# Optimization experiments

Measured on AMD Instinct MI355X. Metric: run time of the kernel, lower is better.

The kernel has to match this reference:

```python
import jax, jax.numpy as jnp
import numpy as np

B, N, DIM = 4, 1024, 768
H, HD = 12, DIM // 12
GP = 49
MLP = 3072


def _layernorm(x, w, b, eps=1e-5):
    mu = x.mean(axis=-1, keepdims=True)
    var = ((x - mu) ** 2).mean(axis=-1, keepdims=True)
    return (x - mu) * jax.lax.rsqrt(var + eps) * w + b


def setup_inputs() -> dict:
    key = jax.random.key(0)
    ks = jax.random.split(key, 12)
    s = 0.02
    return {
        "x": jax.random.normal(ks[0], (B, N, DIM), jnp.float32),
        "ln1_w": jnp.ones((DIM,), jnp.float32),
        "ln1_b": jnp.zeros((DIM,), jnp.float32),
        "qkv_w": jax.random.normal(ks[1], (DIM, 3 * DIM), jnp.float32) * s,
        "qkv_b": jnp.zeros((3 * DIM,), jnp.float32),
        "proj_w": jax.random.normal(ks[2], (DIM, DIM), jnp.float32) * s,
        "proj_b": jnp.zeros((DIM,), jnp.float32),
        "gp_w": jax.random.normal(ks[3], (GP, DIM), jnp.float32) * s,  # nn.Linear(dim, gp_num).weight, shape (gp_num, dim)
        "alpha": jax.random.normal(ks[4], (1, H, 1, 1), jnp.float32),
        "ln2_w": jnp.ones((DIM,), jnp.float32),
        "ln2_b": jnp.zeros((DIM,), jnp.float32),
        "ff1_w": jax.random.normal(ks[5], (DIM, MLP), jnp.float32) * s,
        "ff1_b": jnp.zeros((MLP,), jnp.float32),
        "ff2_w": jax.random.normal(ks[6], (MLP, DIM), jnp.float32) * s,
        "ff2_b": jnp.zeros((DIM,), jnp.float32),
    }


def reference(x, ln1_w, ln1_b, qkv_w, qkv_b, proj_w, proj_b, gp_w, alpha,
              ln2_w, ln2_b, ff1_w, ff1_b, ff2_w, ff2_b):
    b, n, _ = x.shape
    # --- attention branch ---
    xn = _layernorm(x, ln1_w, ln1_b)
    qkv = xn @ qkv_w + qkv_b                                 # [b,n,3*dim]
    q, k, v = jnp.split(qkv, 3, axis=-1)
    to_heads = lambda t: t.reshape(b, n, H, HD).transpose(0, 2, 1, 3)  # [b,h,n,hd]
    q, k, v = to_heads(q), to_heads(k), to_heads(v)
    scale = HD ** -0.5
    attn = jnp.einsum('bhnd,bhmd->bhnm', q, k) * scale       # raw scores
    # group weights: view (gp_num, dim) -> (h, gp_num, hd) (row-major, same as torch .view)
    gp = gp_w.reshape(H, GP, HD)
    gw = jnp.einsum('bhnd,hmd->bhnm', v, gp)                 # [b,h,n,gp]
    gw = jax.nn.gelu(gw, approximate=False)
    gw = jax.nn.softmax(gw, axis=-1)
    gw = jnp.einsum('bhnm,bhkm->bhnk', gw, gw)               # [b,h,n,n]
    attn = jax.nn.softmax(attn * gw, axis=-1)
    a = jax.nn.sigmoid(alpha)
    attn = (1.0 - a) * attn + a * gw
    attn = attn / (attn.sum(axis=2, keepdims=True) + 1e-8)   # note: dim=2 (column renorm), faithful to source
    out = jnp.einsum('bhnm,bhmd->bhnd', attn, v)
    out = out.transpose(0, 2, 1, 3).reshape(b, n, DIM)
    out = out @ proj_w + proj_b
    x = out + x
    # --- FFN branch ---
    xn = _layernorm(x, ln2_w, ln2_b)
    hdn = jax.nn.gelu(xn @ ff1_w + ff1_b, approximate=False)
    x = (hdn @ ff2_w + ff2_b) + x
    return x
```

## Files before the change

kernel.cpp:

```cpp
#include <hip/hip_runtime.h>
#include <hip/hip_bf16.h>
#include <math.h>

#define DEVI __device__ __forceinline__

typedef __bf16 bf16x8 __attribute__((ext_vector_type(8)));
typedef float f32x4 __attribute__((ext_vector_type(4)));
typedef unsigned int u32x4 __attribute__((ext_vector_type(4)));
typedef float f32x4v __attribute__((ext_vector_type(4)));
typedef unsigned short u16;

DEVI u16 f2bf(float f) {
    __hip_bfloat16 h = __float2bfloat16(f);
    return __builtin_bit_cast(u16, h);
}
DEVI float bf2f(u16 u) {
    unsigned int x = ((unsigned int)u) << 16;
    return __builtin_bit_cast(float, x);
}
DEVI float gelu_f(float x) {
    float y = 0.7978845608f * (x + 0.044715f * x * x * x);
    float e = __expf(2.f * y);
    float t = 1.f - 2.f / (e + 1.f);
    return 0.5f * x * (1.f + t);
}
DEVI float sigm(float x) { return 1.f / (1.f + __expf(-x)); }

DEVI bf16x8 ldfrag(const u16* p) {
    return __builtin_bit_cast(bf16x8, *reinterpret_cast<const u32x4*>(p));
}

DEVI void gload_lds16(const u16* g, u16* l) {
    __builtin_amdgcn_global_load_lds(
        (const __attribute__((address_space(1))) void*)g,
        (__attribute__((address_space(3))) void*)l, 16, 0, 0);
}

DEVI void stage8(const u16* gbase, long long stride, u16* lds, int lane) {
    int r = lane >> 3;
    int kg = (lane & 7) ^ r;
    gload_lds16(gbase + (long long)r * stride + kg * 8, lds);
}
DEVI bf16x8 fragsw(const u16* tile, int rr, int k) {
    return ldfrag(&tile[rr * 64 + ((k ^ (rr & 7)) << 3)]);
}

__global__ __launch_bounds__(256) void zero_k(float* __restrict__ p) {
    p[(long long)blockIdx.x * 256 + threadIdx.x] = 0.f;
}

__global__ __launch_bounds__(256) void tcast_k(const float* __restrict__ in, u16* __restrict__ out,
                                               int R, int C) {
    __shared__ float tile[32][33];
    int c0 = blockIdx.x * 32, r0 = blockIdx.y * 32;
    for (int ry = threadIdx.y; ry < 32; ry += 8)
        tile[ry][threadIdx.x] = in[(long long)(r0 + ry) * C + c0 + threadIdx.x];
    __syncthreads();
    for (int cy = threadIdx.y; cy < 32; cy += 8)
        out[(long long)(c0 + cy) * R + r0 + threadIdx.x] = f2bf(tile[threadIdx.x][cy]);
}

__global__ __launch_bounds__(256) void ln_k(const float* __restrict__ parts, int nparts, long long pstride,
                                            const float* __restrict__ bias2, const float* __restrict__ in2,
                                            const float* __restrict__ w, const float* __restrict__ b,
                                            u16* __restrict__ outbf, float* __restrict__ x1out) {
    int row = blockIdx.x;
    long long ro = (long long)row * 768;
    __shared__ float lds1[4], lds2[4];
    float v[3];
    float s = 0.f, sq = 0.f;
#pragma unroll
    for (int j = 0; j < 3; j++) {
        int c = threadIdx.x + j * 256;
        float x = 0.f;
        for (int p = 0; p < nparts; p++) x += parts[p * pstride + ro + c];
        if (bias2) x += bias2[c];
        if (in2) x += in2[ro + c];
        v[j] = x; s += x; sq += x * x;
    }
    if (x1out) {
#pragma unroll
        for (int j = 0; j < 3; j++) x1out[ro + threadIdx.x + j * 256] = v[j];
    }
    for (int off = 32; off; off >>= 1) { s += __shfl_down(s, off); sq += __shfl_down(sq, off); }
    int wid = threadIdx.x >> 6;
    if ((threadIdx.x & 63) == 0) { lds1[wid] = s; lds2[wid] = sq; }
    __syncthreads();
    s = lds1[0] + lds1[1] + lds1[2] + lds1[3];
    sq = lds2[0] + lds2[1] + lds2[2] + lds2[3];
    float mu = s * (1.f / 768.f);
    float var = sq * (1.f / 768.f) - mu * mu;
    float rs = rsqrtf(var + 1e-5f);
#pragma unroll
    for (int j = 0; j < 3; j++) {
        int c = threadIdx.x + j * 256;
        outbf[ro + c] = f2bf((v[j] - mu) * rs * w[c] + b[c]);
    }
}

struct GemmP {
    const u16* A; const u16* B;
    float* outF; u16* outB;
    const float* bias;
    u16* qh; u16* kh; u16* vh;
    int K, lda, ldb, ldc;
    long long pstride;
    int epi;
    int splits;
};

__global__ __launch_bounds__(256) void gemm_bt4(GemmP p) {
    __shared__ u16 As[128 * 64];
    __shared__ u16 Bs[128 * 64];
    const int tid = threadIdx.x, lane = tid & 63, wave = tid >> 6;
    const int l16 = lane & 15, qd = lane >> 4;
    const int bn0 = blockIdx.x * 128, bm0 = blockIdx.y * 128;
    const int wm0 = (wave >> 1) * 64, wn0 = (wave & 1) * 64;
    const int kc = p.K / p.splits;
    const int kbeg = blockIdx.z * kc, kend = kbeg + kc;
    f32x4 acc[4][4] = {};
    for (int k0 = kbeg; k0 < kend; k0 += 64) {
        __syncthreads();
#pragma unroll
        for (int t = 0; t < 4; t++) {
            int rowg = wave * 32 + t * 8;
            stage8(p.A + (long long)(bm0 + rowg) * p.lda + k0, p.lda, As + rowg * 64, lane);
            stage8(p.B + (long long)(bn0 + rowg) * p.ldb + k0, p.ldb, Bs + rowg * 64, lane);
        }
        __syncthreads();
#pragma unroll
        for (int s = 0; s < 2; s++) {
            bf16x8 af[4], bv[4];
#pragma unroll
            for (int i = 0; i < 4; i++) af[i] = fragsw(As, wm0 + i * 16 + l16, s * 4 + qd);
#pragma unroll
            for (int j = 0; j < 4; j++) bv[j] = fragsw(Bs, wn0 + j * 16 + l16, s * 4 + qd);
#pragma unroll
            for (int i = 0; i < 4; i++)
#pragma unroll
                for (int j = 0; j < 4; j++)
                    acc[i][j] = __builtin_amdgcn_mfma_f32_16x16x32_bf16(af[i], bv[j], acc[i][j], 0, 0, 0);
        }
    }
#pragma unroll
    for (int i = 0; i < 4; i++)
#pragma unroll
        for (int j = 0; j < 4; j++)
#pragma unroll
            for (int r = 0; r < 4; r++) {
                int row = bm0 + wm0 + i * 16 + qd * 4 + r;
                int col = bn0 + wn0 + j * 16 + l16;
                float v = acc[i][j][r];
                if (p.epi == 0) {
                    p.outF[(long long)blockIdx.z * p.pstride + (long long)row * p.ldc + col] = v;
                } else if (p.epi == 2) {
                    p.outB[(long long)row * p.ldc + col] = f2bf(gelu_f(v + p.bias[col]));
                } else {
                    v += p.bias[col];
                    int sect = col / 768, cc = col % 768;
                    int h = cc >> 6, d = cc & 63;
                    int b = row >> 10, n = row & 1023;
                    long long o = ((long long)(b * 12 + h) * 1024 + n) * 64 + d;
                    if (sect == 0) p.qh[o] = f2bf(v * 0.125f);
                    else if (sect == 1) p.kh[o] = f2bf(v);
                    else p.vh[o] = f2bf(v);
                }
            }
}

__global__ __launch_bounds__(256) void gpcast_k(const float* __restrict__ gp_w, u16* __restrict__ gpB) {
    int h = blockIdx.x;
    for (int i = threadIdx.x; i < 4096; i += 256) {
        int m = i >> 6, d = i & 63;
        float v = (m < 49) ? gp_w[h * 3136 + m * 64 + d] : 0.f;
        gpB[h * 4096 + i] = f2bf(v);
    }
}

__global__ __launch_bounds__(256) void gw0m_k(const u16* __restrict__ vh, const u16* __restrict__ gpB,
                                              u16* __restrict__ gwn) {
    __shared__ u16 As[64 * 64];
    __shared__ u16 Bs[64 * 64];
    const int tid = threadIdx.x, lane = tid & 63, wave = tid >> 6;
    const int l16 = lane & 15, qd = lane >> 4;
    const int z = blockIdx.y, n0 = blockIdx.x * 64, h = z % 12;
    const u16* vz = vh + ((long long)z * 1024 + n0) * 64;
    const u16* gz = gpB + h * 4096;
#pragma unroll
    for (int t = 0; t < 2; t++) {
        int rowg = wave * 16 + t * 8;
        stage8(vz + (long long)rowg * 64, 64, As + rowg * 64, lane);
        stage8(gz + (long long)rowg * 64, 64, Bs + rowg * 64, lane);
    }
    __syncthreads();
    f32x4 acc[4] = {};
#pragma unroll
    for (int s = 0; s < 2; s++) {
        bf16x8 af = fragsw(As, wave * 16 + l16, s * 4 + qd);
#pragma unroll
        for (int j = 0; j < 4; j++) {
            bf16x8 bv = fragsw(Bs, j * 16 + l16, s * 4 + qd);
            acc[j] = __builtin_amdgcn_mfma_f32_16x16x32_bf16(af, bv, acc[j], 0, 0, 0);
        }
    }
    float ex[4][4];
#pragma unroll
    for (int r = 0; r < 4; r++) {
        float mx = -1e30f;
        float gv[4];
#pragma unroll
        for (int j = 0; j < 4; j++) {
            int col = j * 16 + l16;
            float g = gelu_f(acc[j][r]);
            gv[j] = g;
            if (col < 49) mx = fmaxf(mx, g);
            else gv[j] = -1e30f;
        }
        mx = fmaxf(mx, __shfl_xor(mx, 1)); mx = fmaxf(mx, __shfl_xor(mx, 2));
        mx = fmaxf(mx, __shfl_xor(mx, 4)); mx = fmaxf(mx, __shfl_xor(mx, 8));
        float s = 0.f;
#pragma unroll
        for (int j = 0; j < 4; j++) {
            int col = j * 16 + l16;
            float e = (col < 49) ? __expf(gv[j] - mx) : 0.f;
            ex[r][j] = e;
            s += e;
        }
        s += __shfl_xor(s, 1); s += __shfl_xor(s, 2);
        s += __shfl_xor(s, 4); s += __shfl_xor(s, 8);
        float inv = 1.f / s;
        int row = wave * 16 + qd * 4 + r;
        long long o = ((long long)z * 1024 + n0 + row) * 64;
#pragma unroll
        for (int j = 0; j < 4; j++)
            gwn[o + j * 16 + l16] = f2bf(ex[r][j] * inv);
    }
}

__global__ __launch_bounds__(256) void attn_tg4(const u16* __restrict__ qh, const u16* __restrict__ kh,
                                                const u16* __restrict__ gwn, u16* __restrict__ e,
                                                float* __restrict__ rowsumE) {
    __shared__ u16 As[128 * 64];
    __shared__ u16 Bs[128 * 64];
    const int tid = threadIdx.x, lane = tid & 63, wave = tid >> 6;
    const int l16 = lane & 15, qd = lane >> 4;
    const int bn0 = blockIdx.x * 128, bm0 = blockIdx.y * 128, z = blockIdx.z;
    const int wm0 = (wave >> 1) * 64, wn0 = (wave & 1) * 64;
    const u16* qz = qh + (long long)z * 65536;
    const u16* kz = kh + (long long)z * 65536;
    const u16* gz = gwn + (long long)z * 65536;
    f32x4 accS[4][4] = {};
    f32x4 accG[4][4] = {};
#pragma unroll
    for (int t = 0; t < 4; t++) {
        int rowg = wave * 32 + t * 8;
        stage8(qz + (long long)(bm0 + rowg) * 64, 64, As + rowg * 64, lane);
        stage8(kz + (long long)(bn0 + rowg) * 64, 64, Bs + rowg * 64, lane);
    }
    __syncthreads();
#pragma unroll
    for (int s = 0; s < 2; s++) {
        bf16x8 af[4], bv[4];
#pragma unroll
        for (int i = 0; i < 4; i++) af[i] = fragsw(As, wm0 + i * 16 + l16, s * 4 + qd);
#pragma unroll
        for (int j = 0; j < 4; j++) bv[j] = fragsw(Bs, wn0 + j * 16 + l16, s * 4 + qd);
#pragma unroll
        for (int i = 0; i < 4; i++)
#pragma unroll
            for (int j = 0; j < 4; j++)
                accS[i][j] = __builtin_amdgcn_mfma_f32_16x16x32_bf16(af[i], bv[j], accS[i][j], 0, 0, 0);
    }
    __syncthreads();
#pragma unroll
    for (int t = 0; t < 4; t++) {
        int rowg = wave * 32 + t * 8;
        stage8(gz + (long long)(bm0 + rowg) * 64, 64, As + rowg * 64, lane);
        stage8(gz + (long long)(bn0 + rowg) * 64, 64, Bs + rowg * 64, lane);
    }
    __syncthreads();
#pragma unroll
    for (int s = 0; s < 2; s++) {
        bf16x8 af[4], bv[4];
#pragma unroll
        for (int i = 0; i < 4; i++) af[i] = fragsw(As, wm0 + i * 16 + l16, s * 4 + qd);
#pragma unroll
        for (int j = 0; j < 4; j++) bv[j] = fragsw(Bs, wn0 + j * 16 + l16, s * 4 + qd);
#pragma unroll
        for (int i = 0; i < 4; i++)
#pragma unroll
            for (int j = 0; j < 4; j++)
                accG[i][j] = __builtin_amdgcn_mfma_f32_16x16x32_bf16(af[i], bv[j], accG[i][j], 0, 0, 0);
    }
    long long zoff = (long long)z * 1048576;
#pragma unroll
    for (int i = 0; i < 4; i++)
#pragma unroll
        for (int r = 0; r < 4; r++) {
            int row = bm0 + wm0 + i * 16 + qd * 4 + r;
            float rs = 0.f;
#pragma unroll
            for (int j = 0; j < 4; j++) {
                int col = bn0 + wn0 + j * 16 + l16;
                float ev = __expf(accS[i][j][r] * accG[i][j][r]);
                e[zoff + (long long)row * 1024 + col] = f2bf(ev);
                rs += ev;
            }
            rs += __shfl_xor(rs, 1); rs += __shfl_xor(rs, 2);
            rs += __shfl_xor(rs, 4); rs += __shfl_xor(rs, 8);
            if (l16 == 0) atomicAdd(&rowsumE[z * 1024 + row], rs);
        }
}

__global__ __launch_bounds__(256) void combine2_k(const u16* __restrict__ gwn, const float* __restrict__ alpha,
                                                  float* __restrict__ colsum) {
    int z = blockIdx.x, h = z % 12;
    int j = threadIdx.x & 63, part = threadIdx.x >> 6;
    __shared__ float lds[4][64];
    __shared__ float Sl[64];
    float s = 0.f;
    for (int i = 0; i < 256; i++)
        s += bf2f(gwn[((long long)z * 1024 + part * 256 + i) * 64 + j]);
    lds[part][j] = s;
    __syncthreads();
    if (threadIdx.x < 64)
        Sl[threadIdx.x] = lds[0][threadIdx.x] + lds[1][threadIdx.x] + lds[2][threadIdx.x] + lds[3][threadIdx.x];
    __syncthreads();
    float a = sigm(alpha[h]);
    for (int m = threadIdx.x; m < 1024; m += 256) {
        const u16* g = gwn + ((long long)z * 1024 + m) * 64;
        float dot = 0.f;
#pragma unroll 8
        for (int jj = 0; jj < 64; jj++) dot += bf2f(g[jj]) * Sl[jj];
        colsum[z * 1024 + m] = a * dot;
    }
}

__global__ __launch_bounds__(256) void colsumE_k(const u16* __restrict__ e, const float* __restrict__ rowsumE,
                                                 const float* __restrict__ alpha, float* __restrict__ colsum) {
    int m = blockIdx.x * 256 + threadIdx.x;
    int n0 = blockIdx.y * 128;
    int z = blockIdx.z, h = z % 12;
    float a = sigm(alpha[h]);
    const u16* p = e + (long long)z * 1048576;
    const float* rs = rowsumE + z * 1024;
    float s = 0.f;
    for (int n = n0; n < n0 + 128; n++) s += bf2f(p[(long long)n * 1024 + m]) * (1.f / rs[n]);
    atomicAdd(&colsum[z * 1024 + m], (1.f - a) * s);
}

__global__ __launch_bounds__(256) void vpt_k(const u16* __restrict__ vh, const float* __restrict__ colsum,
                                             u16* __restrict__ vpt) {
    int z = blockIdx.y, m0 = blockIdx.x * 64;
    __shared__ float ts[64 * 65];
    int mi = threadIdx.x >> 6, d = threadIdx.x & 63;
    for (int rr = 0; rr < 16; rr++) {
        int row = rr * 4 + mi;
        ts[row * 65 + d] = bf2f(vh[((long long)z * 1024 + m0 + row) * 64 + d]);
    }
    __syncthreads();
    int mj = threadIdx.x & 63, d0 = threadIdx.x >> 6;
    for (int rr = 0; rr < 16; rr++) {
        int dd = rr * 4 + d0;
        float cs = colsum[z * 1024 + m0 + mj] + 1e-8f;
        vpt[((long long)z * 64 + dd) * 1024 + m0 + mj] = f2bf(ts[mj * 65 + dd] / cs);
    }
}

__global__ __launch_bounds__(256) void wgemm_k(const u16* __restrict__ gwn, const u16* __restrict__ vpt,
                                               float* __restrict__ Wt) {
    int z = blockIdx.y, n0 = blockIdx.x * 128;
    __shared__ u16 gs[128 * 64];
    __shared__ u16 vs2[64 * 128];
    for (int i = threadIdx.x; i < 128 * 64; i += 256) {
        int nn = i >> 6, j = i & 63;
        gs[i] = gwn[((long long)z * 1024 + n0 + nn) * 64 + j];
        int d = i >> 7, n2 = i & 127;
        vs2[i] = vpt[((long long)z * 64 + d) * 1024 + n0 + n2];
    }
    __syncthreads();
    int j = threadIdx.x & 63, dg = threadIdx.x >> 6;
    float acc[16] = {};
    for (int nn = 0; nn < 128; nn++) {
        float g = bf2f(gs[nn * 64 + j]);
#pragma unroll
        for (int i = 0; i < 16; i++) acc[i] += g * bf2f(vs2[(dg * 16 + i) * 128 + nn]);
    }
#pragma unroll
    for (int i = 0; i < 16; i++)
        atomicAdd(&Wt[((long long)z * 64 + dg * 16 + i) * 64 + j], acc[i]);
}

__global__ __launch_bounds__(256) void wtcast_k(const float* __restrict__ Wt, u16* __restrict__ WtB) {
    long long i = (long long)blockIdx.x * 256 + threadIdx.x;
    WtB[i] = f2bf(Wt[i]);
}

__global__ __launch_bounds__(256) void attn_out4(const u16* __restrict__ e, const u16* __restrict__ vpt,
                                                 const u16* __restrict__ gwn, const u16* __restrict__ WtB,
                                                 const float* __restrict__ rowsumE,
                                                 const float* __restrict__ alpha, u16* __restrict__ out) {
    __shared__ u16 As[64 * 64];
    __shared__ u16 Bs[64 * 64];
    const int tid = threadIdx.x, lane = tid & 63, wave = tid >> 6;
    const int l16 = lane & 15, qd = lane >> 4;
    const int bm0 = blockIdx.x * 64, z = blockIdx.y;
    const int h = z % 12, b = z / 12;
    const u16* Pz = e + (long long)z * 1048576;
    const u16* vz = vpt + (long long)z * 65536;
    const int wr = wave * 16;
    f32x4 accP[4] = {};
    f32x4 accG[4] = {};
    for (int k0 = 0; k0 < 1024; k0 += 64) {
        __syncthreads();
#pragma unroll
        for (int t = 0; t < 2; t++) {
            int rowg = wave * 16 + t * 8;
            stage8(Pz + (long long)(bm0 + rowg) * 1024 + k0, 1024, As + rowg * 64, lane);
            stage8(vz + (long long)rowg * 1024 + k0, 1024, Bs + rowg * 64, lane);
        }
        __syncthreads();
#pragma unroll
        for (int s = 0; s < 2; s++) {
            bf16x8 af = fragsw(As, wr + l16, s * 4 + qd);
#pragma unroll
            for (int j = 0; j < 4; j++) {
                bf16x8 bv = fragsw(Bs, j * 16 + l16, s * 4 + qd);
                accP[j] = __builtin_amdgcn_mfma_f32_16x16x32_bf16(af, bv, accP[j], 0, 0, 0);
            }
        }
    }
    const u16* gz = gwn + (long long)z * 65536;
    const u16* wz = WtB + (long long)z * 4096;
    __syncthreads();
#pragma unroll
    for (int t = 0; t < 2; t++) {
        int rowg = wave * 16 + t * 8;
        stage8(gz + (long long)(bm0 + rowg) * 64, 64, As + rowg * 64, lane);
        stage8(wz + (long long)rowg * 64, 64, Bs + rowg * 64, lane);
    }
    __syncthreads();
#pragma unroll
    for (int s = 0; s < 2; s++) {
        bf16x8 af = fragsw(As, wr + l16, s * 4 + qd);
#pragma unroll
        for (int j = 0; j < 4; j++) {
            bf16x8 bv = fragsw(Bs, j * 16 + l16, s * 4 + qd);
            accG[j] = __builtin_amdgcn_mfma_f32_16x16x32_bf16(af, bv, accG[j], 0, 0, 0);
        }
    }
    float a = sigm(alpha[h]);
#pragma unroll
    for (int r = 0; r < 4; r++) {
        int n = bm0 + wr + qd * 4 + r;
        float sc = (1.f - a) / rowsumE[z * 1024 + n];
#pragma unroll
        for (int j = 0; j < 4; j++) {
            int d = j * 16 + l16;
            float v = sc * accP[j][r] + a * accG[j][r];
            out[((long long)(b * 1024 + n)) * 768 + h * 64 + d] = f2bf(v);
        }
    }
}

__global__ __launch_bounds__(256) void fuse2_k(const float* __restrict__ parts, long long pstride4,
                                               const float* __restrict__ bias, const float* __restrict__ x1,
                                               float* __restrict__ outp) {
    long long i4 = (long long)blockIdx.x * 256 + threadIdx.x;
    int c4 = (int)(i4 % 192);
    const f32x4v* p0 = (const f32x4v*)parts;
    f32x4v v = p0[i4] + p0[pstride4 + i4];
    f32x4v bb = ((const f32x4v*)bias)[c4];
    f32x4v xx = ((const f32x4v*)x1)[i4];
    ((f32x4v*)outp)[i4] = v + bb + xx;
}

extern "C" void kernel_launch(void* const* d_in, const int* in_sizes, int n_in,
                              void* d_out, int out_size, void* d_ws, size_t ws_size,
                              hipStream_t stream) {
    const float* x      = (const float*)d_in[0];
    const float* ln1_w  = (const float*)d_in[1];
    const float* ln1_b  = (const float*)d_in[2];
    const float* qkv_w  = (const float*)d_in[3];
    const float* qkv_b  = (const float*)d_in[4];
    const float* proj_w = (const float*)d_in[5];
    const float* proj_b = (const float*)d_in[6];
    const float* gp_w   = (const float*)d_in[7];
    const float* alpha  = (const float*)d_in[8];
    const float* ln2_w  = (const float*)d_in[9];
    const float* ln2_b  = (const float*)d_in[10];
    const float* ff1_w  = (const float*)d_in[11];
    const float* ff1_b  = (const float*)d_in[12];
    const float* ff2_w  = (const float*)d_in[13];
    const float* ff2_b  = (const float*)d_in[14];

    char* w = (char*)d_ws;
    size_t off = 0;
    auto alloc = [&](size_t bytes) { size_t r = off; off += (bytes + 255) & ~(size_t)255; return r; };

    u16*   xn_bf   = (u16*)(w + alloc(4096LL * 768 * 2));
    u16*   wqkv_t  = (u16*)(w + alloc(2304LL * 768 * 2));
    u16*   wproj_t = (u16*)(w + alloc(768LL * 768 * 2));
    u16*   wff1_t  = (u16*)(w + alloc(3072LL * 768 * 2));
    u16*   wff2_t  = (u16*)(w + alloc(768LL * 3072 * 2));
    u16*   gpB     = (u16*)(w + alloc(12LL * 64 * 64 * 2));
    u16*   qh      = (u16*)(w + alloc(48LL * 1024 * 64 * 2));
    u16*   kh      = (u16*)(w + alloc(48LL * 1024 * 64 * 2));
    u16*   vh      = (u16*)(w + alloc(48LL * 1024 * 64 * 2));
    u16*   gwn     = (u16*)(w + alloc(48LL * 1024 * 64 * 2));
    u16*   ebuf    = (u16*)(w + alloc(48LL * 1024 * 1024 * 2));
    float* rowsumE = (float*)(w + alloc(48LL * 1024 * 4));
    float* Wt      = (float*)(w + alloc(48LL * 64 * 64 * 4));
    u16*   WtB     = (u16*)(w + alloc(48LL * 64 * 64 * 2));
    float* colsum  = (float*)(w + alloc(48LL * 1024 * 4));
    u16*   vpt     = (u16*)(w + alloc(48LL * 64 * 1024 * 2));
    float* x1      = (float*)(w + alloc(4096LL * 768 * 4));
    u16*   attn_o  = (u16*)(w + alloc(4096LL * 768 * 2));
    u16*   xn2     = (u16*)(w + alloc(4096LL * 768 * 2));
    float* projP = (float*)ebuf;
    u16*   hmid  = (u16*)((char*)ebuf + 2 * 4096LL * 768 * 4);
    float* ff2P  = (float*)((char*)ebuf + 2 * 4096LL * 768 * 4 + 4096LL * 3072 * 2);

    dim3 blk(256);
    const long long PS = 4096LL * 768;

    tcast_k<<<dim3(72, 24), dim3(32, 8), 0, stream>>>(qkv_w, wqkv_t, 768, 2304);
    tcast_k<<<dim3(24, 24), dim3(32, 8), 0, stream>>>(proj_w, wproj_t, 768, 768);
    tcast_k<<<dim3(96, 24), dim3(32, 8), 0, stream>>>(ff1_w, wff1_t, 768, 3072);
    tcast_k<<<dim3(24, 96), dim3(32, 8), 0, stream>>>(ff2_w, wff2_t, 3072, 768);
    gpcast_k<<<dim3(12), blk, 0, stream>>>(gp_w, gpB);

    ln_k<<<dim3(4096), blk, 0, stream>>>(x, 1, 0, nullptr, nullptr, ln1_w, ln1_b, xn_bf, nullptr);

    {
        GemmP p = {xn_bf, wqkv_t, nullptr, nullptr, qkv_b, qh, kh, vh, 768, 768, 768, 0, 0, 4, 1};
        gemm_bt4<<<dim3(18, 32, 1), blk, 0, stream>>>(p);
    }

    gw0m_k<<<dim3(16, 48), blk, 0, stream>>>(vh, gpB, gwn);

    zero_k<<<dim3(192), blk, 0, stream>>>(rowsumE);
    attn_tg4<<<dim3(8, 8, 48), blk, 0, stream>>>(qh, kh, gwn, ebuf, rowsumE);

    combine2_k<<<dim3(48), blk, 0, stream>>>(gwn, alpha, colsum);
    colsumE_k<<<dim3(4, 8, 48), blk, 0, stream>>>(ebuf, rowsumE, alpha, colsum);

    vpt_k<<<dim3(16, 48), blk, 0, stream>>>(vh, colsum, vpt);

    zero_k<<<dim3(768), blk, 0, stream>>>(Wt);
    wgemm_k<<<dim3(8, 48), blk, 0, stream>>>(gwn, vpt, Wt);
    wtcast_k<<<dim3(768), blk, 0, stream>>>(Wt, WtB);

    attn_out4<<<dim3(16, 48), blk, 0, stream>>>(ebuf, vpt, gwn, WtB, rowsumE, alpha, attn_o);

    {
        GemmP p = {attn_o, wproj_t, projP, nullptr, nullptr, nullptr, nullptr, nullptr,
                   768, 768, 768, 768, PS, 0, 2};
        gemm_bt4<<<dim3(6, 32, 2), blk, 0, stream>>>(p);
    }

    ln_k<<<dim3(4096), blk, 0, stream>>>(projP, 2, PS, proj_b, x, ln2_w, ln2_b, xn2, x1);

    {
        GemmP p = {xn2, wff1_t, nullptr, hmid, ff1_b, nullptr, nullptr, nullptr,
                   768, 768, 768, 3072, 0, 2, 1};
        gemm_bt4<<<dim3(24, 32, 1), blk, 0, stream>>>(p);
    }

    {
        GemmP p = {hmid, wff2_t, ff2P, nullptr, nullptr, nullptr, nullptr, nullptr,
                   3072, 3072, 3072, 768, PS, 0, 2};
        gemm_bt4<<<dim3(6, 32, 2), blk, 0, stream>>>(p);
    }

    fuse2_k<<<dim3(3072), blk, 0, stream>>>(ff2P, PS / 4, ff2_b, x1, (float*)d_out);
}
```

Baseline: 480.9 us.

## Shrink GEMM tiles, fold zero-fill and cast kernels, vectorize column sums

Several separate changes are bundled. The bf16 GEMM moves from 128x128 tiles with four waves to 64x128 tiles with two waves, which doubles the block count per launch. The zero-fill kernels for rowsumE and Wt are removed: the zeroing now happens inside ln_k and gw0m_k, and the fp32-to-bf16 Wt cast is done while staging inside attn_out4, which drops three launches. colsumE_k now reads 16-byte vectors and reduces through shared memory before issuing atomics, cutting scalar loads and atomic traffic. The tradeoffs are more duplicated B-tile loads per output in the GEMM and uncoalesced scalar fp32 reads for Wt in attn_out4.

```diff
diff --git a/kernel.cpp b/kernel.cpp
--- a/kernel.cpp
+++ b/kernel.cpp
@@ -43,10 +43,6 @@
 }
 DEVI bf16x8 fragsw(const u16* tile, int rr, int k) {
     return ldfrag(&tile[rr * 64 + ((k ^ (rr & 7)) << 3)]);
-}
-
-__global__ __launch_bounds__(256) void zero_k(float* __restrict__ p) {
-    p[(long long)blockIdx.x * 256 + threadIdx.x] = 0.f;
 }
 
 __global__ __launch_bounds__(256) void tcast_k(const float* __restrict__ in, u16* __restrict__ out,
@@ -63,8 +59,10 @@
 __global__ __launch_bounds__(256) void ln_k(const float* __restrict__ parts, int nparts, long long pstride,
                                             const float* __restrict__ bias2, const float* __restrict__ in2,
                                             const float* __restrict__ w, const float* __restrict__ b,
-                                            u16* __restrict__ outbf, float* __restrict__ x1out) {
+                                            u16* __restrict__ outbf, float* __restrict__ x1out,
+                                            float* __restrict__ zfill) {
     int row = blockIdx.x;
+    if (zfill && row < 192) zfill[row * 256 + threadIdx.x] = 0.f;
     long long ro = (long long)row * 768;
     __shared__ float lds1[4], lds2[4];
     float v[3];
@@ -109,13 +107,13 @@
     int splits;
 };
 
-__global__ __launch_bounds__(256) void gemm_bt4(GemmP p) {
-    __shared__ u16 As[128 * 64];
+__global__ __launch_bounds__(128) void gemm_bt2(GemmP p) {
+    __shared__ u16 As[64 * 64];
     __shared__ u16 Bs[128 * 64];
     const int tid = threadIdx.x, lane = tid & 63, wave = tid >> 6;
     const int l16 = lane & 15, qd = lane >> 4;
-    const int bn0 = blockIdx.x * 128, bm0 = blockIdx.y * 128;
-    const int wm0 = (wave >> 1) * 64, wn0 = (wave & 1) * 64;
+    const int bn0 = blockIdx.x * 128, bm0 = blockIdx.y * 64;
+    const int wn0 = wave * 64;
     const int kc = p.K / p.splits;
     const int kbeg = blockIdx.z * kc, kend = kbeg + kc;
     f32x4 acc[4][4] = {};
@@ -125,6 +123,10 @@
         for (int t = 0; t < 4; t++) {
             int rowg = wave * 32 + t * 8;
             stage8(p.A + (long long)(bm0 + rowg) * p.lda + k0, p.lda, As + rowg * 64, lane);
+        }
+#pragma unroll
+        for (int t = 0; t < 8; t++) {
+            int rowg = wave * 64 + t * 8;
             stage8(p.B + (long long)(bn0 + rowg) * p.ldb + k0, p.ldb, Bs + rowg * 64, lane);
         }
         __syncthreads();
@@ -132,7 +134,7 @@
         for (int s = 0; s < 2; s++) {
             bf16x8 af[4], bv[4];
 #pragma unroll
-            for (int i = 0; i < 4; i++) af[i] = fragsw(As, wm0 + i * 16 + l16, s * 4 + qd);
+            for (int i = 0; i < 4; i++) af[i] = fragsw(As, i * 16 + l16, s * 4 + qd);
 #pragma unroll
             for (int j = 0; j < 4; j++) bv[j] = fragsw(Bs, wn0 + j * 16 + l16, s * 4 + qd);
 #pragma unroll
@@ -148,7 +150,7 @@
         for (int j = 0; j < 4; j++)
 #pragma unroll
             for (int r = 0; r < 4; r++) {
-                int row = bm0 + wm0 + i * 16 + qd * 4 + r;
+                int row = bm0 + i * 16 + qd * 4 + r;
                 int col = bn0 + wn0 + j * 16 + l16;
                 float v = acc[i][j][r];
                 if (p.epi == 0) {
@@ -178,7 +180,11 @@
 }
 
 __global__ __launch_bounds__(256) void gw0m_k(const u16* __restrict__ vh, const u16* __restrict__ gpB,
-                                              u16* __restrict__ gwn) {
+                                              u16* __restrict__ gwn, float* __restrict__ Wt) {
+    {
+        long long zi = ((long long)blockIdx.y * 16 + blockIdx.x) * 256 + threadIdx.x;
+        Wt[zi] = 0.f;
+    }
     __shared__ u16 As[64 * 64];
     __shared__ u16 Bs[64 * 64];
     const int tid = threadIdx.x, lane = tid & 63, wave = tid >> 6;
@@ -338,15 +344,35 @@
 
 __global__ __launch_bounds__(256) void colsumE_k(const u16* __restrict__ e, const float* __restrict__ rowsumE,
                                                  const float* __restrict__ alpha, float* __restrict__ colsum) {
-    int m = blockIdx.x * 256 + threadIdx.x;
+    int z = blockIdx.x, h = z % 12;
     int n0 = blockIdx.y * 128;
-    int z = blockIdx.z, h = z % 12;
-    float a = sigm(alpha[h]);
+    int grp = threadIdx.x & 127;
+    int half = threadIdx.x >> 7;
     const u16* p = e + (long long)z * 1048576;
     const float* rs = rowsumE + z * 1024;
-    float s = 0.f;
-    for (int n = n0; n < n0 + 128; n++) s += bf2f(p[(long long)n * 1024 + m]) * (1.f / rs[n]);
-    atomicAdd(&colsum[z * 1024 + m], (1.f - a) * s);
+    float acc[8] = {};
+    for (int n = n0 + half * 64; n < n0 + half * 64 + 64; n++) {
+        unsigned int rw[4];
+        *reinterpret_cast<u32x4*>(rw) = *reinterpret_cast<const u32x4*>(&p[(long long)n * 1024 + grp * 8]);
+        float inv = 1.f / rs[n];
+#pragma unroll
+        for (int q = 0; q < 4; q++) {
+            float lo = __builtin_bit_cast(float, rw[q] << 16);
+            float hi = __builtin_bit_cast(float, rw[q] & 0xffff0000u);
+            acc[2 * q] += lo * inv;
+            acc[2 * q + 1] += hi * inv;
+        }
+    }
+    __shared__ float part[2][128][8];
+#pragma unroll
+    for (int j = 0; j < 8; j++) part[half][grp][j] = acc[j];
+    __syncthreads();
+    if (half == 0) {
+        float a = sigm(alpha[h]);
+#pragma unroll
+        for (int j = 0; j < 8; j++)
+            atomicAdd(&colsum[z * 1024 + grp * 8 + j], (1.f - a) * (part[0][grp][j] + part[1][grp][j]));
+    }
 }
 
 __global__ __launch_bounds__(256) void vpt_k(const u16* __restrict__ vh, const float* __restrict__ colsum,
@@ -391,13 +417,8 @@
         atomicAdd(&Wt[((long long)z * 64 + dg * 16 + i) * 64 + j], acc[i]);
 }
 
-__global__ __launch_bounds__(256) void wtcast_k(const float* __restrict__ Wt, u16* __restrict__ WtB) {
-    long long i = (long long)blockIdx.x * 256 + threadIdx.x;
-    WtB[i] = f2bf(Wt[i]);
-}
-
 __global__ __launch_bounds__(256) void attn_out4(const u16* __restrict__ e, const u16* __restrict__ vpt,
-                                                 const u16* __restrict__ gwn, const u16* __restrict__ WtB,
+                                                 const u16* __restrict__ gwn, const float* __restrict__ Wt,
                                                  const float* __restrict__ rowsumE,
                                                  const float* __restrict__ alpha, u16* __restrict__ out) {
     __shared__ u16 As[64 * 64];
@@ -431,13 +452,22 @@
         }
     }
     const u16* gz = gwn + (long long)z * 65536;
-    const u16* wz = WtB + (long long)z * 4096;
+    const float* wz = Wt + (long long)z * 4096;
     __syncthreads();
 #pragma unroll
     for (int t = 0; t < 2; t++) {
         int rowg = wave * 16 + t * 8;
         stage8(gz + (long long)(bm0 + rowg) * 64, 64, As + rowg * 64, lane);
-        stage8(wz + (long long)rowg * 64, 64, Bs + rowg * 64, lane);
+    }
+    {
+        int row = tid >> 2, c0 = (tid & 3) * 16;
+        const float* wrow = wz + row * 64;
+#pragma unroll
+        for (int j0 = 0; j0 < 16; j0++) {
+            int j = c0 + j0;
+            int pos = (((j >> 3) ^ (row & 7)) << 3) | (j & 7);
+            Bs[row * 64 + pos] = f2bf(wrow[j]);
+        }
     }
     __syncthreads();
 #pragma unroll
@@ -511,7 +541,6 @@
     u16*   ebuf    = (u16*)(w + alloc(48LL * 1024 * 1024 * 2));
     float* rowsumE = (float*)(w + alloc(48LL * 1024 * 4));
     float* Wt      = (float*)(w + alloc(48LL * 64 * 64 * 4));
-    u16*   WtB     = (u16*)(w + alloc(48LL * 64 * 64 * 2));
     float* colsum  = (float*)(w + alloc(48LL * 1024 * 4));
     u16*   vpt     = (u16*)(w + alloc(48LL * 64 * 1024 * 2));
     float* x1      = (float*)(w + alloc(4096LL * 768 * 4));
@@ -522,6 +551,7 @@
     float* ff2P  = (float*)((char*)ebuf + 2 * 4096LL * 768 * 4 + 4096LL * 3072 * 2);
 
     dim3 blk(256);
+    dim3 blk2(128);
     const long long PS = 4096LL * 768;
 
     tcast_k<<<dim3(72, 24), dim3(32, 8), 0, stream>>>(qkv_w, wqkv_t, 768, 2304);
@@ -530,47 +560,44 @@
     tcast_k<<<dim3(24, 96), dim3(32, 8), 0, stream>>>(ff2_w, wff2_t, 3072, 768);
     gpcast_k<<<dim3(12), blk, 0, stream>>>(gp_w, gpB);
 
-    ln_k<<<dim3(4096), blk, 0, stream>>>(x, 1, 0, nullptr, nullptr, ln1_w, ln1_b, xn_bf, nullptr);
+    ln_k<<<dim3(4096), blk, 0, stream>>>(x, 1, 0, nullptr, nullptr, ln1_w, ln1_b, xn_bf, nullptr, rowsumE);
 
     {
         GemmP p = {xn_bf, wqkv_t, nullptr, nullptr, qkv_b, qh, kh, vh, 768, 768, 768, 0, 0, 4, 1};
-        gemm_bt4<<<dim3(18, 32, 1), blk, 0, stream>>>(p);
-    }
-
-    gw0m_k<<<dim3(16, 48), blk, 0, stream>>>(vh, gpB, gwn);
-
-    zero_k<<<dim3(192), blk, 0, stream>>>(rowsumE);
+        gemm_bt2<<<dim3(18, 64, 1), blk2, 0, stream>>>(p);
+    }
+
+    gw0m_k<<<dim3(16, 48), blk, 0, stream>>>(vh, gpB, gwn, Wt);
+
     attn_tg4<<<dim3(8, 8, 48), blk, 0, stream>>>(qh, kh, gwn, ebuf, rowsumE);
 
     combine2_k<<<dim3(48), blk, 0, stream>>>(gwn, alpha, colsum);
-    colsumE_k<<<dim3(4, 8, 48), blk, 0, stream>>>(ebuf, rowsumE, alpha, colsum);
+    colsumE_k<<<dim3(48, 8), blk, 0, stream>>>(ebuf, rowsumE, alpha, colsum);
 
     vpt_k<<<dim3(16, 48), blk, 0, stream>>>(vh, colsum, vpt);
 
-    zero_k<<<dim3(768), blk, 0, stream>>>(Wt);
     wgemm_k<<<dim3(8, 48), blk, 0, stream>>>(gwn, vpt, Wt);
-    wtcast_k<<<dim3(768), blk, 0, stream>>>(Wt, WtB);
-
-    attn_out4<<<dim3(16, 48), blk, 0, stream>>>(ebuf, vpt, gwn, WtB, rowsumE, alpha, attn_o);
+
+    attn_out4<<<dim3(16, 48), blk, 0, stream>>>(ebuf, vpt, gwn, Wt, rowsumE, alpha, attn_o);
 
     {
         GemmP p = {attn_o, wproj_t, projP, nullptr, nullptr, nullptr, nullptr, nullptr,
                    768, 768, 768, 768, PS, 0, 2};
-        gemm_bt4<<<dim3(6, 32, 2), blk, 0, stream>>>(p);
-    }
-
-    ln_k<<<dim3(4096), blk, 0, stream>>>(projP, 2, PS, proj_b, x, ln2_w, ln2_b, xn2, x1);
+        gemm_bt2<<<dim3(6, 64, 2), blk2, 0, stream>>>(p);
+    }
+
+    ln_k<<<dim3(4096), blk, 0, stream>>>(projP, 2, PS, proj_b, x, ln2_w, ln2_b, xn2, x1, nullptr);
 
     {
         GemmP p = {xn2, wff1_t, nullptr, hmid, ff1_b, nullptr, nullptr, nullptr,
                    768, 768, 768, 3072, 0, 2, 1};
-        gemm_bt4<<<dim3(24, 32, 1), blk, 0, stream>>>(p);
+        gemm_bt2<<<dim3(24, 64, 1), blk2, 0, stream>>>(p);
     }
 
     {
         GemmP p = {hmid, wff2_t, ff2P, nullptr, nullptr, nullptr, nullptr, nullptr,
                    3072, 3072, 3072, 768, PS, 0, 2};
-        gemm_bt4<<<dim3(6, 32, 2), blk, 0, stream>>>(p);
+        gemm_bt2<<<dim3(6, 64, 2), blk2, 0, stream>>>(p);
     }
 
     fuse2_k<<<dim3(3072), blk, 0, stream>>>(ff2P, PS / 4, ff2_b, x1, (float*)d_out);
```

After: 487.3 us. About the same (+1.3%).
